# Kernel tuning notes

Measured on AMD Instinct MI355X. Metric: run time of the kernel, lower is better.

Reference implementation:

```python
import jax, jax.numpy as jnp
import numpy as np

SIGNAL_LEN = 2048
N_WAVELETS = 32
TWO_PI = 2.0 * np.pi


def _encoder(x, W1, b1, W2, b2, W3, b3, W4, b4):
    B = x.shape[0]
    h = x.reshape(B, -1)                      # (B, 4096)
    h = jax.nn.relu(h @ W1.T + b1)            # (B, 1024)
    h = jax.nn.relu(h @ W2.T + b2)            # (B, 512)
    h = jax.nn.relu(h @ W3.T + b3)            # (B, 256)
    return h @ W4.T + b4                      # (B, n_wavelets*5)


def _synthesize(params):
    # params: (B, N_WAVELETS, 5)
    A = params[..., 0]                                    # (B, N)
    t0 = jax.nn.sigmoid(params[..., 1]) * SIGNAL_LEN      # (B, N)
    f = jax.nn.sigmoid(params[..., 2]) * 0.5              # (B, N)
    sigma = jax.nn.sigmoid(params[..., 3]) * 200.0 + 2.0  # (B, N)
    phi = params[..., 4]                                  # (B, N)

    t = jnp.arange(SIGNAL_LEN, dtype=params.dtype)        # (T,)
    dt = t[None, None, :] - t0[..., None]                 # (B, N, T)
    g = (A[..., None]
         * jnp.exp(-(dt * dt) / (2.0 * sigma[..., None] ** 2))
         * jnp.cos(TWO_PI * f[..., None] * dt + phi[..., None]))  # (B, N, T)
    sig = jnp.sum(g, axis=1)                              # (B, T)
    # both channels receive the identical wavelet sum (as in the torch code)
    return jnp.stack([sig, sig], axis=1)                  # (B, 2, T)


def setup_inputs() -> dict:
    key = jax.random.key(0)
    ks = jax.random.split(key, 9)
    B = 4096
    def w(k, shape, fan_in):
        return jax.random.normal(k, shape, dtype=jnp.float32) / np.sqrt(fan_in)
    return {
        "x": jax.random.normal(ks[0], (B, 2, SIGNAL_LEN), dtype=jnp.float32),
        "W1": w(ks[1], (1024, 4096), 4096), "b1": jnp.zeros((1024,), jnp.float32),
        "W2": w(ks[2], (512, 1024), 1024),  "b2": jnp.zeros((512,), jnp.float32),
        "W3": w(ks[3], (256, 512), 512),    "b3": jnp.zeros((256,), jnp.float32),
        "W4": w(ks[4], (N_WAVELETS * 5, 256), 256), "b4": jnp.zeros((N_WAVELETS * 5,), jnp.float32),
    }


def reference(x, W1, b1, W2, b2, W3, b3, W4, b4):
    B = x.shape[0]
    params = _encoder(x, W1, b1, W2, b2, W3, b3, W4, b4).reshape(B, N_WAVELETS, 5)
    return _synthesize(params)  # (B, 2, SIGNAL_LEN)
```

## Files before the change

### kernel.cpp

```cpp
#include <hip/hip_runtime.h>


#define SIGNAL_LEN 2048
#define NWAV 32

typedef _Float16 f16x8 __attribute__((ext_vector_type(8)));
typedef _Float16 f16x4 __attribute__((ext_vector_type(4)));
typedef float    f32x4 __attribute__((ext_vector_type(4)));

__device__ __forceinline__ void load16_lds(const _Float16* g, _Float16* l) {
  __builtin_amdgcn_global_load_lds((const __attribute__((address_space(1))) void*)g,
                                   (__attribute__((address_space(3))) void*)l,
                                   16, 0, 0);
}

struct HL { _Float16 h, l; };
__device__ __forceinline__ HL split_one(float a) {
  HL r;
  r.h = (_Float16)a;
  r.l = (_Float16)((a - (float)r.h) * 4096.0f);
  return r;
}

__global__ void split_x(const float4* __restrict__ src, f16x4* __restrict__ dh,
                        f16x4* __restrict__ dl) {
  int i = blockIdx.x * 256 + threadIdx.x;
  float4 v = src[i];
  float a[4] = {v.x, v.y, v.z, v.w};
  f16x4 h, l;
#pragma unroll
  for (int j = 0; j < 4; j++) {
    HL r = split_one(a[j]);
    h[j] = r.h;
    l[j] = r.l;
  }
  dh[i] = h;
  dl[i] = l;
}

__global__ void split_weights(const float* __restrict__ W1, const float* __restrict__ W2,
                              const float* __restrict__ W3, const float* __restrict__ W4,
                              const float* __restrict__ b4,
                              f16x4* __restrict__ W1h, f16x4* __restrict__ W1l,
                              f16x4* __restrict__ W2h, f16x4* __restrict__ W2l,
                              f16x4* __restrict__ W3h, f16x4* __restrict__ W3l,
                              f16x4* __restrict__ W4h, f16x4* __restrict__ W4l,
                              float* __restrict__ b4p) {
  const int blk = blockIdx.x;
  const int tid = threadIdx.x;
  if (blk < 4736) {
    const float4* src;
    f16x4 *dh, *dl;
    int i;
    if (blk < 4096) {
      src = (const float4*)W1; dh = W1h; dl = W1l; i = blk * 256 + tid;
    } else if (blk < 4608) {
      src = (const float4*)W2; dh = W2h; dl = W2l; i = (blk - 4096) * 256 + tid;
    } else {
      src = (const float4*)W3; dh = W3h; dl = W3l; i = (blk - 4608) * 256 + tid;
    }
    float4 v = src[i];
    float a[4] = {v.x * 256.0f, v.y * 256.0f, v.z * 256.0f, v.w * 256.0f};
    f16x4 h, l;
#pragma unroll
    for (int j = 0; j < 4; j++) {
      HL r = split_one(a[j]);
      h[j] = r.h;
      l[j] = r.l;
    }
    dh[i] = h;
    dl[i] = l;
  } else if (blk < 4800) {
    int i = (blk - 4736) * 256 + tid;
    int i4 = i << 2;
    int row = i4 >> 8;
    f16x4 h, l;
#pragma unroll
    for (int j = 0; j < 4; j++) {
      float a = (row < 160) ? W4[i4 + j] * 256.0f : 0.0f;
      HL r = split_one(a);
      h[j] = r.h;
      l[j] = r.l;
    }
    W4h[i] = h;
    W4l[i] = l;
  } else {
    b4p[tid] = (tid < 160) ? b4[tid] : 0.0f;
  }
}

template <int TM, int N, int K, bool RELU, bool SPLIT_OUT>
__global__ void __launch_bounds__(256, 2)
gemm_f16x2(const _Float16* __restrict__ Ah, const _Float16* __restrict__ Al,
           const _Float16* __restrict__ Bh, const _Float16* __restrict__ Bl,
           const float* __restrict__ bias,
           _Float16* __restrict__ Ch, _Float16* __restrict__ Cl,
           float* __restrict__ Cf) {
  constexpr int IM = TM / 32;
  __shared__ __align__(16) _Float16 sAh[TM * 32];
  __shared__ __align__(16) _Float16 sAl[TM * 32];
  __shared__ __align__(16) _Float16 sBh[64 * 32];
  __shared__ __align__(16) _Float16 sBl[64 * 32];

  const int tid = threadIdx.x;
  const int lane = tid & 63;
  const int w = tid >> 6;
  const int wm = w >> 1, wn = w & 1;
  const int m0 = blockIdx.y * TM;
  const int n0 = blockIdx.x * 64;

  const int srow = lane >> 2;
  const int schunk = ((lane & 3) - (lane >> 3)) & 3;
  const int sk8 = schunk * 8;

  const size_t aOff = (size_t)(m0 + 16 * w + srow) * K + sk8;
  const _Float16* gAh0 = Ah + aOff;
  const _Float16* gAl0 = Al + aOff;
  const size_t bOff = (size_t)(n0 + 16 * w + srow) * K + sk8;
  const _Float16* gBh0 = Bh + bOff;
  const _Float16* gBl0 = Bl + bOff;

  _Float16* lAh0 = sAh + w * 512;
  _Float16* lAl0 = sAl + w * 512;
  _Float16* lAh1 = sAh + 2048 + w * 512;
  _Float16* lAl1 = sAl + 2048 + w * 512;
  _Float16* lBh = sBh + w * 512;
  _Float16* lBl = sBl + w * 512;

  const int fr = lane & 15;
  const int fq = lane >> 4;
  const int fslot8 = (4 * fr + ((fq + (fr >> 1)) & 3)) * 8;

  f32x4 acc1[IM][2], acc2[IM][2];
#pragma unroll
  for (int i = 0; i < IM; i++)
#pragma unroll
    for (int j = 0; j < 2; j++) {
      acc1[i][j] = 0.0f;
      acc2[i][j] = 0.0f;
    }

  for (int kt = 0; kt < K; kt += 32) {
    load16_lds(gAh0 + kt, lAh0);
    load16_lds(gAl0 + kt, lAl0);
    if (TM == 128) {
      load16_lds(gAh0 + (size_t)64 * K + kt, lAh1);
      load16_lds(gAl0 + (size_t)64 * K + kt, lAl1);
    }
    load16_lds(gBh0 + kt, lBh);
    load16_lds(gBl0 + kt, lBl);
    __syncthreads();

    f16x8 fAh[IM], fAl[IM], fBh[2], fBl[2];
#pragma unroll
    for (int im = 0; im < IM; im++) {
      fAh[im] = *(const f16x8*)(sAh + (wm * IM + im) * 512 + fslot8);
      fAl[im] = *(const f16x8*)(sAl + (wm * IM + im) * 512 + fslot8);
    }
#pragma unroll
    for (int in = 0; in < 2; in++) {
      fBh[in] = *(const f16x8*)(sBh + (wn * 2 + in) * 512 + fslot8);
      fBl[in] = *(const f16x8*)(sBl + (wn * 2 + in) * 512 + fslot8);
    }
#pragma unroll
    for (int im = 0; im < IM; im++) {
#pragma unroll
      for (int in = 0; in < 2; in++) {
        acc1[im][in] = __builtin_amdgcn_mfma_f32_16x16x32_f16(fAh[im], fBh[in], acc1[im][in], 0, 0, 0);
        acc2[im][in] = __builtin_amdgcn_mfma_f32_16x16x32_f16(fAh[im], fBl[in], acc2[im][in], 0, 0, 0);
        acc2[im][in] = __builtin_amdgcn_mfma_f32_16x16x32_f16(fAl[im], fBh[in], acc2[im][in], 0, 0, 0);
      }
    }
    __syncthreads();
  }

  const int quad = lane >> 4;
#pragma unroll
  for (int in = 0; in < 2; in++) {
    const int n = n0 + wn * 32 + in * 16 + fr;
    const float bv = bias[n];
#pragma unroll
    for (int im = 0; im < IM; im++) {
#pragma unroll
      for (int r = 0; r < 4; r++) {
        const int m = m0 + wm * (TM / 2) + im * 16 + quad * 4 + r;
        float c = (acc1[im][in][r] + acc2[im][in][r] * (1.0f / 4096.0f)) * (1.0f / 256.0f) + bv;
        if (RELU) c = fmaxf(c, 0.0f);
        const size_t off = (size_t)m * N + n;
        if (SPLIT_OUT) {
          HL rr = split_one(c);
          Ch[off] = rr.h;
          Cl[off] = rr.l;
        } else {
          Cf[off] = c;
        }
      }
    }
  }
}

__global__ void __launch_bounds__(256)
synth(const float* __restrict__ P, float* __restrict__ out) {
  __shared__ float sA[NWAV], sT0[NWAV], sF[NWAV], sC[NWAV], sPh[NWAV], sSg[NWAV];
  const int b = blockIdx.x;
  const int tid = threadIdx.x;
  if (tid < NWAV) {
    const float* q = P + (size_t)b * 256 + tid * 5;
    const float L2E = 1.44269504088896340736f;
    float A = q[0], p1 = q[1], p2 = q[2], p3 = q[3], p4 = q[4];
    float s1 = 1.0f / (1.0f + exp2f(-p1 * L2E));
    float s2 = 1.0f / (1.0f + exp2f(-p2 * L2E));
    float s3 = 1.0f / (1.0f + exp2f(-p3 * L2E));
    float sg = s3 * 200.0f + 2.0f;
    sA[tid] = A;
    sT0[tid] = s1 * 2048.0f;
    sF[tid] = s2 * 0.5f;
    sC[tid] = -L2E / (2.0f * sg * sg);
    sPh[tid] = p4 * 0.15915494309189535f;
    sSg[tid] = sg;
  }
  __syncthreads();

  const float t0f = (float)(tid * 8);
  const int wlo = (tid & ~63) * 8;
  float acc[8];
#pragma unroll
  for (int i = 0; i < 8; i++) acc[i] = 0.0f;

  for (int wv = 0; wv < NWAV; wv++) {
    const float t0 = sT0[wv], sg = sSg[wv];
    if (t0 + 5.0f * sg < (float)wlo || t0 - 5.0f * sg > (float)(wlo + 511)) continue;
    const float A = sA[wv], fr = sF[wv], cn = sC[wv], ph = sPh[wv];
#pragma unroll
    for (int i = 0; i < 8; i++) {
      float dt = (t0f + (float)i) - t0;
      float e = exp2f(dt * dt * cn);
      float r = fr * dt + ph;
      r -= floorf(r);
      float cs = __builtin_amdgcn_cosf(r);
      acc[i] += A * e * cs;
    }
  }

  float* o = out + (size_t)b * (2 * SIGNAL_LEN) + tid * 8;
  float4 v0 = make_float4(acc[0], acc[1], acc[2], acc[3]);
  float4 v1 = make_float4(acc[4], acc[5], acc[6], acc[7]);
  *(float4*)(o) = v0;
  *(float4*)(o + 4) = v1;
  *(float4*)(o + SIGNAL_LEN) = v0;
  *(float4*)(o + SIGNAL_LEN + 4) = v1;
}

extern "C" void kernel_launch(void* const* d_in, const int* in_sizes, int n_in,
                              void* d_out, int out_size, void* d_ws, size_t ws_size,
                              hipStream_t stream) {
  (void)in_sizes; (void)n_in; (void)out_size; (void)ws_size;
  const float* X  = (const float*)d_in[0];
  const float* W1 = (const float*)d_in[1];
  const float* b1 = (const float*)d_in[2];
  const float* W2 = (const float*)d_in[3];
  const float* b2 = (const float*)d_in[4];
  const float* W3 = (const float*)d_in[5];
  const float* b3 = (const float*)d_in[6];
  const float* W4 = (const float*)d_in[7];
  const float* b4 = (const float*)d_in[8];
  float* out = (float*)d_out;

  char* p = (char*)d_ws;
  auto take = [&](size_t bytes) -> char* {
    char* r = p;
    p += (bytes + 255) & ~(size_t)255;
    return r;
  };
  _Float16* Xh  = (_Float16*)take((size_t)4096 * 4096 * 2);
  _Float16* Xl  = (_Float16*)take((size_t)4096 * 4096 * 2);
  _Float16* W1h = (_Float16*)take((size_t)1024 * 4096 * 2);
  _Float16* W1l = (_Float16*)take((size_t)1024 * 4096 * 2);
  _Float16* H1h = (_Float16*)take((size_t)4096 * 1024 * 2);
  _Float16* H1l = (_Float16*)take((size_t)4096 * 1024 * 2);
  _Float16* W2h = (_Float16*)take((size_t)512 * 1024 * 2);
  _Float16* W2l = (_Float16*)take((size_t)512 * 1024 * 2);
  _Float16* H2h = (_Float16*)take((size_t)4096 * 512 * 2);
  _Float16* H2l = (_Float16*)take((size_t)4096 * 512 * 2);
  _Float16* W3h = (_Float16*)take((size_t)256 * 512 * 2);
  _Float16* W3l = (_Float16*)take((size_t)256 * 512 * 2);
  _Float16* H3h = (_Float16*)take((size_t)4096 * 256 * 2);
  _Float16* H3l = (_Float16*)take((size_t)4096 * 256 * 2);
  _Float16* W4h = (_Float16*)take((size_t)256 * 256 * 2);
  _Float16* W4l = (_Float16*)take((size_t)256 * 256 * 2);
  float*    b4p = (float*)take(256 * 4);
  float*    Pp  = (float*)take((size_t)4096 * 256 * 4);

  split_x<<<16384, 256, 0, stream>>>((const float4*)X, (f16x4*)Xh, (f16x4*)Xl);
  split_weights<<<4801, 256, 0, stream>>>(W1, W2, W3, W4, b4,
                                          (f16x4*)W1h, (f16x4*)W1l, (f16x4*)W2h, (f16x4*)W2l,
                                          (f16x4*)W3h, (f16x4*)W3l, (f16x4*)W4h, (f16x4*)W4l, b4p);

  gemm_f16x2<128, 1024, 4096, true, true><<<dim3(16, 32), 256, 0, stream>>>(
      Xh, Xl, W1h, W1l, b1, H1h, H1l, nullptr);
  gemm_f16x2<64, 512, 1024, true, true><<<dim3(8, 64), 256, 0, stream>>>(
      H1h, H1l, W2h, W2l, b2, H2h, H2l, nullptr);
  gemm_f16x2<64, 256, 512, true, true><<<dim3(4, 64), 256, 0, stream>>>(
      H2h, H2l, W3h, W3l, b3, H3h, H3l, nullptr);
  gemm_f16x2<64, 256, 256, false, false><<<dim3(4, 64), 256, 0, stream>>>(
      H3h, H3l, W4h, W4l, b4p, nullptr, nullptr, Pp);

  synth<<<4096, 256, 0, stream>>>(Pp, out);
}
```

Baseline: 414.8 us.

## Double-buffer LDS in split-f16 GEMM and widen N tiles

Rewrites the split-precision GEMM to use two LDS buffers, issuing the next K-tile's global-to-LDS loads before computing on the current tile, with one barrier per iteration instead of two. It also adds a TN template parameter so layers 1 and 2 use 128-wide N tiles, halving their grid in N. The aim is to hide global load latency behind MFMA work and raise data reuse per block. The cost is more LDS per block, which may reduce occupancy, and fewer blocks for the first two GEMMs.

```diff
diff --git a/kernel.cpp b/kernel.cpp
--- a/kernel.cpp
+++ b/kernel.cpp
@@ -89,100 +89,107 @@
   }
 }
 
-template <int TM, int N, int K, bool RELU, bool SPLIT_OUT>
+template <int TM, int TN, int N, int K, bool RELU, bool SPLIT_OUT>
 __global__ void __launch_bounds__(256, 2)
-gemm_f16x2(const _Float16* __restrict__ Ah, const _Float16* __restrict__ Al,
-           const _Float16* __restrict__ Bh, const _Float16* __restrict__ Bl,
-           const float* __restrict__ bias,
-           _Float16* __restrict__ Ch, _Float16* __restrict__ Cl,
-           float* __restrict__ Cf) {
-  constexpr int IM = TM / 32;
-  __shared__ __align__(16) _Float16 sAh[TM * 32];
-  __shared__ __align__(16) _Float16 sAl[TM * 32];
-  __shared__ __align__(16) _Float16 sBh[64 * 32];
-  __shared__ __align__(16) _Float16 sBl[64 * 32];
+gemm_db(const _Float16* __restrict__ Ah, const _Float16* __restrict__ Al,
+        const _Float16* __restrict__ Bh, const _Float16* __restrict__ Bl,
+        const float* __restrict__ bias,
+        _Float16* __restrict__ Ch, _Float16* __restrict__ Cl,
+        float* __restrict__ Cf) {
+  constexpr int AM = TM / 32;
+  constexpr int BN = TN / 32;
+  constexpr int AU = TM / 8;
+  constexpr int TU = (TM + TN) / 8;
+  constexpr int UPW = TU / 4;
+  constexpr int NK = K / 32;
+
+  __shared__ __align__(16) _Float16 s[2][(TM + TN) * 64];
 
   const int tid = threadIdx.x;
   const int lane = tid & 63;
   const int w = tid >> 6;
   const int wm = w >> 1, wn = w & 1;
   const int m0 = blockIdx.y * TM;
-  const int n0 = blockIdx.x * 64;
+  const int n0 = blockIdx.x * TN;
 
   const int srow = lane >> 2;
-  const int schunk = ((lane & 3) - (lane >> 3)) & 3;
-  const int sk8 = schunk * 8;
-
-  const size_t aOff = (size_t)(m0 + 16 * w + srow) * K + sk8;
-  const _Float16* gAh0 = Ah + aOff;
-  const _Float16* gAl0 = Al + aOff;
-  const size_t bOff = (size_t)(n0 + 16 * w + srow) * K + sk8;
-  const _Float16* gBh0 = Bh + bOff;
-  const _Float16* gBl0 = Bl + bOff;
-
-  _Float16* lAh0 = sAh + w * 512;
-  _Float16* lAl0 = sAl + w * 512;
-  _Float16* lAh1 = sAh + 2048 + w * 512;
-  _Float16* lAl1 = sAl + 2048 + w * 512;
-  _Float16* lBh = sBh + w * 512;
-  _Float16* lBl = sBl + w * 512;
+  const int sk8 = (((lane & 3) - (lane >> 3)) & 3) * 8;
+
+  const _Float16* gb[UPW];
+  int lo[UPW];
+#pragma unroll
+  for (int i = 0; i < UPW; ++i) {
+    const int u = w * UPW + i;
+    if (u < AU) {
+      const int g = u >> 1, hl = u & 1;
+      gb[i] = (hl ? Al : Ah) + (size_t)(m0 + g * 16 + srow) * K + sk8;
+    } else {
+      const int ub = u - AU;
+      const int g = ub >> 1, hl = ub & 1;
+      gb[i] = (hl ? Bl : Bh) + (size_t)(n0 + g * 16 + srow) * K + sk8;
+    }
+    lo[i] = u * 512;
+  }
 
   const int fr = lane & 15;
   const int fq = lane >> 4;
   const int fslot8 = (4 * fr + ((fq + (fr >> 1)) & 3)) * 8;
 
-  f32x4 acc1[IM][2], acc2[IM][2];
-#pragma unroll
-  for (int i = 0; i < IM; i++)
-#pragma unroll
-    for (int j = 0; j < 2; j++) {
+  f32x4 acc1[AM][BN], acc2[AM][BN];
+#pragma unroll
+  for (int i = 0; i < AM; i++)
+#pragma unroll
+    for (int j = 0; j < BN; j++) {
       acc1[i][j] = 0.0f;
       acc2[i][j] = 0.0f;
     }
 
-  for (int kt = 0; kt < K; kt += 32) {
-    load16_lds(gAh0 + kt, lAh0);
-    load16_lds(gAl0 + kt, lAl0);
-    if (TM == 128) {
-      load16_lds(gAh0 + (size_t)64 * K + kt, lAh1);
-      load16_lds(gAl0 + (size_t)64 * K + kt, lAl1);
-    }
-    load16_lds(gBh0 + kt, lBh);
-    load16_lds(gBl0 + kt, lBl);
+#pragma unroll
+  for (int i = 0; i < UPW; ++i) load16_lds(gb[i], &s[0][lo[i]]);
+
+  for (int kt = 0; kt < NK; ++kt) {
+    const int cur = kt & 1;
     __syncthreads();
 
-    f16x8 fAh[IM], fAl[IM], fBh[2], fBl[2];
-#pragma unroll
-    for (int im = 0; im < IM; im++) {
-      fAh[im] = *(const f16x8*)(sAh + (wm * IM + im) * 512 + fslot8);
-      fAl[im] = *(const f16x8*)(sAl + (wm * IM + im) * 512 + fslot8);
-    }
-#pragma unroll
-    for (int in = 0; in < 2; in++) {
-      fBh[in] = *(const f16x8*)(sBh + (wn * 2 + in) * 512 + fslot8);
-      fBl[in] = *(const f16x8*)(sBl + (wn * 2 + in) * 512 + fslot8);
-    }
-#pragma unroll
-    for (int im = 0; im < IM; im++) {
-#pragma unroll
-      for (int in = 0; in < 2; in++) {
+    if (kt + 1 < NK) {
+      const int kofs = (kt + 1) * 32;
+#pragma unroll
+      for (int i = 0; i < UPW; ++i) load16_lds(gb[i] + kofs, &s[cur ^ 1][lo[i]]);
+    }
+
+    f16x8 fAh[AM], fAl[AM], fBh[BN], fBl[BN];
+#pragma unroll
+    for (int im = 0; im < AM; ++im) {
+      const int g = wm * AM + im;
+      fAh[im] = *(const f16x8*)(&s[cur][(g * 2 + 0) * 512 + fslot8]);
+      fAl[im] = *(const f16x8*)(&s[cur][(g * 2 + 1) * 512 + fslot8]);
+    }
+#pragma unroll
+    for (int in = 0; in < BN; ++in) {
+      const int g = wn * BN + in;
+      fBh[in] = *(const f16x8*)(&s[cur][TM * 64 + (g * 2 + 0) * 512 + fslot8]);
+      fBl[in] = *(const f16x8*)(&s[cur][TM * 64 + (g * 2 + 1) * 512 + fslot8]);
+    }
+#pragma unroll
+    for (int im = 0; im < AM; ++im) {
+#pragma unroll
+      for (int in = 0; in < BN; ++in) {
         acc1[im][in] = __builtin_amdgcn_mfma_f32_16x16x32_f16(fAh[im], fBh[in], acc1[im][in], 0, 0, 0);
         acc2[im][in] = __builtin_amdgcn_mfma_f32_16x16x32_f16(fAh[im], fBl[in], acc2[im][in], 0, 0, 0);
         acc2[im][in] = __builtin_amdgcn_mfma_f32_16x16x32_f16(fAl[im], fBh[in], acc2[im][in], 0, 0, 0);
       }
     }
-    __syncthreads();
   }
 
   const int quad = lane >> 4;
 #pragma unroll
-  for (int in = 0; in < 2; in++) {
-    const int n = n0 + wn * 32 + in * 16 + fr;
+  for (int in = 0; in < BN; ++in) {
+    const int n = n0 + wn * (TN / 2) + in * 16 + fr;
     const float bv = bias[n];
 #pragma unroll
-    for (int im = 0; im < IM; im++) {
-#pragma unroll
-      for (int r = 0; r < 4; r++) {
+    for (int im = 0; im < AM; ++im) {
+#pragma unroll
+      for (int r = 0; r < 4; ++r) {
         const int m = m0 + wm * (TM / 2) + im * 16 + quad * 4 + r;
         float c = (acc1[im][in][r] + acc2[im][in][r] * (1.0f / 4096.0f)) * (1.0f / 256.0f) + bv;
         if (RELU) c = fmaxf(c, 0.0f);
@@ -296,13 +303,13 @@
                                           (f16x4*)W1h, (f16x4*)W1l, (f16x4*)W2h, (f16x4*)W2l,
                                           (f16x4*)W3h, (f16x4*)W3l, (f16x4*)W4h, (f16x4*)W4l, b4p);
 
-  gemm_f16x2<128, 1024, 4096, true, true><<<dim3(16, 32), 256, 0, stream>>>(
+  gemm_db<128, 128, 1024, 4096, true, true><<<dim3(8, 32), 256, 0, stream>>>(
       Xh, Xl, W1h, W1l, b1, H1h, H1l, nullptr);
-  gemm_f16x2<64, 512, 1024, true, true><<<dim3(8, 64), 256, 0, stream>>>(
+  gemm_db<64, 128, 512, 1024, true, true><<<dim3(4, 64), 256, 0, stream>>>(
       H1h, H1l, W2h, W2l, b2, H2h, H2l, nullptr);
-  gemm_f16x2<64, 256, 512, true, true><<<dim3(4, 64), 256, 0, stream>>>(
+  gemm_db<64, 64, 256, 512, true, true><<<dim3(4, 64), 256, 0, stream>>>(
       H2h, H2l, W3h, W3l, b3, H3h, H3l, nullptr);
-  gemm_f16x2<64, 256, 256, false, false><<<dim3(4, 64), 256, 0, stream>>>(
+  gemm_db<64, 64, 256, 256, false, false><<<dim3(4, 64), 256, 0, stream>>>(
       H3h, H3l, W4h, W4l, b4p, nullptr, nullptr, Pp);
 
   synth<<<4096, 256, 0, stream>>>(Pp, out);
```

Measured after the change: 403.8 us. 1.03x faster.
